# Kernel optimization log

Hardware: AMD Instinct MI355X
Metric: run time of the kernel (lower is better)

The kernel has to match this reference:

```python
import jax, jax.numpy as jnp
import numpy as np

HIDDEN = 2048
HEADS = 16
HEAD_DIM = HIDDEN // HEADS
BATCH = 2
SEQ = 2048


def setup_inputs() -> dict:
    key = jax.random.key(0)
    ks = jax.random.split(key, 9)
    s = 0.02
    return {
        "x": jax.random.normal(ks[0], (BATCH, SEQ, HIDDEN), dtype=jnp.float32),
        "Wq": jax.random.normal(ks[1], (HIDDEN, HIDDEN), dtype=jnp.float32) * s,
        "bq": jax.random.normal(ks[2], (HIDDEN,), dtype=jnp.float32) * s,
        "Wk": jax.random.normal(ks[3], (HIDDEN, HIDDEN), dtype=jnp.float32) * s,
        "bk": jax.random.normal(ks[4], (HIDDEN,), dtype=jnp.float32) * s,
        "Wv": jax.random.normal(ks[5], (HIDDEN, HIDDEN), dtype=jnp.float32) * s,
        "bv": jax.random.normal(ks[6], (HIDDEN,), dtype=jnp.float32) * s,
        "Wo": jax.random.normal(ks[7], (HIDDEN, HIDDEN), dtype=jnp.float32) * s,
        "bo": jax.random.normal(ks[8], (HIDDEN,), dtype=jnp.float32) * s,
    }


def reference(x, Wq, bq, Wk, bk, Wv, bv, Wo, bo):
    B, S, H = x.shape
    # Linear layers: y = x @ W.T + b (torch nn.Linear convention, W:[out,in])
    q = x @ Wq.T + bq
    k = x @ Wk.T + bk
    v = x @ Wv.T + bv
    # [B, S, H] -> [B, nH, S, hd]
    def split_heads(t):
        return t.reshape(B, S, HEADS, HEAD_DIM).transpose(0, 2, 1, 3)
    q, k, v = split_heads(q), split_heads(k), split_heads(v)
    scale = 1.0 / (HEAD_DIM ** 0.5)
    # NOTE: original module applies NO causal mask despite its name; be faithful.
    scores = jnp.einsum('bhqd,bhkd->bhqk', q, k) * scale
    probs = jax.nn.softmax(scores, axis=-1)
    attn = jnp.einsum('bhqk,bhkd->bhqd', probs, v)
    attn = attn.transpose(0, 2, 1, 3).reshape(B, S, H)
    return attn @ Wo.T + bo
```

## Files before the change

kernel.cpp:

```cpp
#include <hip/hip_runtime.h>
#include <hip/hip_bf16.h>
#include <stdint.h>

typedef __bf16 bf16_t;
typedef __attribute__((ext_vector_type(8))) __bf16 bf16x8;
typedef __attribute__((ext_vector_type(4))) float floatx4;

typedef __attribute__((address_space(1))) const unsigned int gu32_t;
typedef __attribute__((address_space(3))) unsigned int lu32_t;

__device__ __forceinline__ void async16(const void* g, void* l) {
    __builtin_amdgcn_global_load_lds((gu32_t*)g, (lu32_t*)l, 16, 0, 0);
}

__device__ __forceinline__ uint32_t pack2(float lo, float hi) {
    union { bf16_t h[2]; uint32_t u; } cv;
    cv.h[0] = (bf16_t)lo; cv.h[1] = (bf16_t)hi;
    return cv.u;
}

__global__ __launch_bounds__(256) void cvt_f32_bf16(const float* __restrict__ in,
                                                    bf16_t* __restrict__ out) {
    int i = (blockIdx.x * 256 + threadIdx.x) * 8;
    float4 a = *(const float4*)(in + i);
    float4 b = *(const float4*)(in + i + 4);
    bf16x8 v;
    v[0] = (bf16_t)a.x; v[1] = (bf16_t)a.y; v[2] = (bf16_t)a.z; v[3] = (bf16_t)a.w;
    v[4] = (bf16_t)b.x; v[5] = (bf16_t)b.y; v[6] = (bf16_t)b.z; v[7] = (bf16_t)b.w;
    *(bf16x8*)(out + i) = v;
}

template <bool OUT_F32, bool BIAS_ROW>
__global__ __launch_bounds__(256) void gemm_bt(const bf16_t* __restrict__ A,
                                               const bf16_t* __restrict__ B,
                                               const float* __restrict__ bias,
                                               const float* __restrict__ bias2,
                                               int nsplit,
                                               float* __restrict__ Cf,
                                               bf16_t* __restrict__ Cb,
                                               int M, int N, int K, int ldc) {
    __shared__ bf16_t As[128 * 64];
    __shared__ bf16_t Bs[128 * 64];
    const int tid = threadIdx.x;
    const int wave = tid >> 6, lane = tid & 63;
    const int quad = lane >> 4, l16 = lane & 15;
    const int wm = (wave >> 1) * 64, wn = (wave & 1) * 64;
    const int tm = blockIdx.x * 128, tn = blockIdx.y * 128;

    floatx4 acc[4][4];
#pragma unroll
    for (int i = 0; i < 4; ++i)
#pragma unroll
        for (int j = 0; j < 4; ++j) acc[i][j] = floatx4{0.f, 0.f, 0.f, 0.f};

    const bf16_t* Abase = A + (size_t)tm * K;
    const bf16_t* Bbase = B + (size_t)tn * K;
    const int sw = l16 & 7;

    for (int kk = 0; kk < K; kk += 64) {
#pragma unroll
        for (int it = 0; it < 4; ++it) {
            int chunk = it * 256 + tid;
            int r = chunk >> 3, c = chunk & 7;
            int c2 = c ^ (r & 7);
            async16(Abase + r * K + kk + c2 * 8, As + (it * 256 + wave * 64) * 8);
            async16(Bbase + r * K + kk + c2 * 8, Bs + (it * 256 + wave * 64) * 8);
        }
        __syncthreads();
#pragma unroll
        for (int ks = 0; ks < 2; ++ks) {
            bf16x8 af[4], bf[4];
#pragma unroll
            for (int mt = 0; mt < 4; ++mt)
                af[mt] = *(const bf16x8*)(As + (wm + mt * 16 + l16) * 64 +
                                          ((ks * 4 + quad) ^ sw) * 8);
#pragma unroll
            for (int nt = 0; nt < 4; ++nt)
                bf[nt] = *(const bf16x8*)(Bs + (wn + nt * 16 + l16) * 64 +
                                          ((ks * 4 + quad) ^ sw) * 8);
#pragma unroll
            for (int mt = 0; mt < 4; ++mt)
#pragma unroll
                for (int nt = 0; nt < 4; ++nt)
                    acc[mt][nt] = __builtin_amdgcn_mfma_f32_16x16x32_bf16(af[mt], bf[nt],
                                                                          acc[mt][nt], 0, 0, 0);
        }
        __syncthreads();
    }
#pragma unroll
    for (int mt = 0; mt < 4; ++mt)
#pragma unroll
        for (int nt = 0; nt < 4; ++nt)
#pragma unroll
            for (int r = 0; r < 4; ++r) {
                int row = tm + wm + mt * 16 + quad * 4 + r;
                int col = tn + wn + nt * 16 + l16;
                float bv = BIAS_ROW ? bias[row]
                                    : (col < nsplit ? bias[col] : bias2[col - nsplit]);
                float v = acc[mt][nt][r] + bv;
                if (OUT_F32) Cf[(size_t)row * ldc + col] = v;
                else Cb[(size_t)row * ldc + col] = (bf16_t)v;
            }
}

__global__ __launch_bounds__(256, 4) void flash_attn(const bf16_t* __restrict__ Qp,
                                                     const bf16_t* __restrict__ Kp,
                                                     const bf16_t* __restrict__ Vt,
                                                     bf16_t* __restrict__ O) {
    __shared__ bf16_t Ks[64 * 128];
    __shared__ bf16_t Vts[128 * 64];
    const int tid = threadIdx.x;
    const int wave = tid >> 6, lane = tid & 63;
    const int quad = lane >> 4, l16 = lane & 15;
    const int QKLD = 4096, T = 4096, S = 2048, HIDO = 2048;
    const float SL2E = 0.088388347688f * 1.44269504089f;

    const int qrow0 = blockIdx.z * S + blockIdx.x * 64;
    const int krow0 = blockIdx.z * S;
    const int hoff = blockIdx.y * 128;
    const int sw = l16 & 7;

    bf16x8 qf[4];
    const bf16_t* qptr = Qp + (size_t)(qrow0 + wave * 16 + l16) * QKLD + hoff;
#pragma unroll
    for (int ks = 0; ks < 4; ++ks) qf[ks] = *(const bf16x8*)(qptr + ks * 32 + quad * 8);

    float m_i = -3.0e38f, l_i = 0.f;
    floatx4 Oacc[8];
#pragma unroll
    for (int dt = 0; dt < 8; ++dt) Oacc[dt] = floatx4{0.f, 0.f, 0.f, 0.f};

    for (int kt = 0; kt < 32; ++kt) {
        int kb = krow0 + kt * 64;
#pragma unroll
        for (int it = 0; it < 4; ++it) {
            int chunk = it * 256 + tid;
            int r = chunk >> 4, c = chunk & 15;
            int c2 = c ^ (r & 7);
            async16(Kp + (size_t)(kb + r) * QKLD + hoff + c2 * 8,
                    Ks + (it * 256 + wave * 64) * 8);
        }
#pragma unroll
        for (int it = 0; it < 4; ++it) {
            int chunk = it * 256 + tid;
            int r = chunk >> 3, c = chunk & 7;
            int c2 = c ^ (r & 7);
            async16(Vt + (size_t)(hoff + r) * T + kb + c2 * 8,
                    Vts + (it * 256 + wave * 64) * 8);
        }
        __syncthreads();

        floatx4 sf[4];
#pragma unroll
        for (int nt = 0; nt < 4; ++nt) sf[nt] = floatx4{0.f, 0.f, 0.f, 0.f};
#pragma unroll
        for (int ks = 0; ks < 4; ++ks) {
#pragma unroll
            for (int nt = 0; nt < 4; ++nt) {
                bf16x8 a = *(const bf16x8*)(Ks + (nt * 16 + l16) * 128 +
                                            ((ks * 4 + quad) ^ sw) * 8);
                sf[nt] = __builtin_amdgcn_mfma_f32_16x16x32_bf16(a, qf[ks], sf[nt], 0, 0, 0);
            }
        }

        float mx = -3.0e38f;
#pragma unroll
        for (int nt = 0; nt < 4; ++nt)
#pragma unroll
            for (int r = 0; r < 4; ++r) mx = fmaxf(mx, sf[nt][r]);
        mx *= SL2E;
        mx = fmaxf(mx, __shfl_xor(mx, 16));
        mx = fmaxf(mx, __shfl_xor(mx, 32));
        float mnew = fmaxf(m_i, mx);
        float alpha = exp2f(m_i - mnew);
        m_i = mnew;

        float rsum = 0.f;
        uint32_t pk[8];
#pragma unroll
        for (int nt = 0; nt < 4; ++nt)
#pragma unroll
            for (int h = 0; h < 2; ++h) {
                float p0 = exp2f(sf[nt][2 * h] * SL2E - mnew);
                float p1 = exp2f(sf[nt][2 * h + 1] * SL2E - mnew);
                rsum += p0 + p1;
                pk[nt * 2 + h] = pack2(p0, p1);
            }
        rsum += __shfl_xor(rsum, 16);
        rsum += __shfl_xor(rsum, 32);
        l_i = l_i * alpha + rsum;

        float aO[4];
#pragma unroll
        for (int r = 0; r < 4; ++r) aO[r] = __shfl(alpha, quad * 4 + r);
#pragma unroll
        for (int dt = 0; dt < 8; ++dt)
#pragma unroll
            for (int r = 0; r < 4; ++r) Oacc[dt][r] *= aO[r];

        const int qsel = quad >> 1;
        const int src0 = (quad & 1) * 32 + l16;
        const int src1 = src0 + 16;
#pragma unroll
        for (int ks2 = 0; ks2 < 2; ++ks2) {
            const int rA = 4 * ks2;
            uint32_t a0 = (uint32_t)__shfl((int)pk[rA + 0], src0);
            uint32_t b0 = (uint32_t)__shfl((int)pk[rA + 2], src0);
            uint32_t a1 = (uint32_t)__shfl((int)pk[rA + 1], src0);
            uint32_t b1 = (uint32_t)__shfl((int)pk[rA + 3], src0);
            uint32_t a2 = (uint32_t)__shfl((int)pk[rA + 0], src1);
            uint32_t b2 = (uint32_t)__shfl((int)pk[rA + 2], src1);
            uint32_t a3 = (uint32_t)__shfl((int)pk[rA + 1], src1);
            uint32_t b3 = (uint32_t)__shfl((int)pk[rA + 3], src1);
            union { uint32_t u[4]; bf16x8 v; } af;
            af.u[0] = qsel ? b0 : a0;
            af.u[1] = qsel ? b1 : a1;
            af.u[2] = qsel ? b2 : a2;
            af.u[3] = qsel ? b3 : a3;
#pragma unroll
            for (int dt = 0; dt < 8; ++dt) {
                bf16x8 b = *(const bf16x8*)(Vts + (dt * 16 + l16) * 64 +
                                            ((ks2 * 4 + quad) ^ sw) * 8);
                Oacc[dt] = __builtin_amdgcn_mfma_f32_16x16x32_bf16(af.v, b, Oacc[dt], 0, 0, 0);
            }
        }
        __syncthreads();
    }
    float linv = 1.0f / l_i;
    float lO[4];
#pragma unroll
    for (int r = 0; r < 4; ++r) lO[r] = __shfl(linv, quad * 4 + r);
#pragma unroll
    for (int dt = 0; dt < 8; ++dt)
#pragma unroll
        for (int r = 0; r < 4; ++r) {
            int row = qrow0 + wave * 16 + quad * 4 + r;
            int col = hoff + dt * 16 + l16;
            O[(size_t)row * HIDO + col] = (bf16_t)(Oacc[dt][r] * lO[r]);
        }
}

extern "C" void kernel_launch(void* const* d_in, const int* in_sizes, int n_in,
                              void* d_out, int out_size, void* d_ws, size_t ws_size,
                              hipStream_t stream) {
    const float* x  = (const float*)d_in[0];
    const float* Wq = (const float*)d_in[1];
    const float* bq = (const float*)d_in[2];
    const float* Wk = (const float*)d_in[3];
    const float* bk = (const float*)d_in[4];
    const float* Wv = (const float*)d_in[5];
    const float* bv = (const float*)d_in[6];
    const float* Wo = (const float*)d_in[7];
    const float* bo = (const float*)d_in[8];
    float* out = (float*)d_out;

    const int T = 4096;
    const int H = 2048;
    bf16_t* ws  = (bf16_t*)d_ws;
    bf16_t* xb  = ws;
    bf16_t* wqb = xb  + (size_t)T * H;
    bf16_t* wkb = wqb + (size_t)H * H;
    bf16_t* wvb = wkb + (size_t)H * H;
    bf16_t* wob = wvb + (size_t)H * H;
    bf16_t* QKb = wob + (size_t)H * H;
    bf16_t* Vtb = QKb + (size_t)T * 2 * H;
    bf16_t* Ab  = Vtb + (size_t)H * T;
    size_t need = (size_t)(Ab + (size_t)T * H - ws) * sizeof(bf16_t);
    if (ws_size < need) return;

    cvt_f32_bf16<<<T * H / 2048, 256, 0, stream>>>(x, xb);
    cvt_f32_bf16<<<H * H / 2048, 256, 0, stream>>>(Wq, wqb);
    cvt_f32_bf16<<<H * H / 2048, 256, 0, stream>>>(Wk, wkb);
    cvt_f32_bf16<<<H * H / 2048, 256, 0, stream>>>(Wv, wvb);
    cvt_f32_bf16<<<H * H / 2048, 256, 0, stream>>>(Wo, wob);

    dim3 gqk(T / 128, 4096 / 128);
    gemm_bt<false, false><<<gqk, 256, 0, stream>>>(xb, wqb, bq, bk, H,
                                                   nullptr, QKb, T, 4096, H, 4096);
    dim3 gv(H / 128, T / 128);
    gemm_bt<false, true><<<gv, 256, 0, stream>>>(wvb, xb, bv, nullptr, 0,
                                                 nullptr, Vtb, H, T, H, T);

    flash_attn<<<dim3(32, 16, 2), 256, 0, stream>>>(QKb, QKb + H, Vtb, Ab);

    dim3 go(T / 128, H / 128);
    gemm_bt<true, false><<<go, 256, 0, stream>>>(Ab, wob, bo, nullptr, H,
                                                 out, nullptr, T, H, H, H);
}
```

Before: 461.1 us.

## Rewrite flash attention with 32x32x16 MFMA, two waves per block, LDS-staged output

The attention kernel switches from 16x16x32 to 32x32x16 bf16 MFMA tiles, with each of two waves owning 32 query rows instead of four waves owning 16. This cuts LDS fragment reads per FLOP and simplifies the softmax reductions and the P-fragment shuffles, which drop to a single xor-32 exchange. The output is now staged through LDS to produce coalesced row stores. The cost is fewer waves per block, larger per-wave register use (occupancy hint changed to 128 threads, 2 blocks per CU), and the same 32 KB of LDS now shared by only two waves, which may hurt latency hiding.

New measurement: 463.0 us. Within noise of the previous version (+0.4%).

```diff
diff --git a/kernel.cpp b/kernel.cpp
--- a/kernel.cpp
+++ b/kernel.cpp
@@ -5,6 +5,7 @@
 typedef __bf16 bf16_t;
 typedef __attribute__((ext_vector_type(8))) __bf16 bf16x8;
 typedef __attribute__((ext_vector_type(4))) float floatx4;
+typedef __attribute__((ext_vector_type(16))) float f32x16;
 
 typedef __attribute__((address_space(1))) const unsigned int gu32_t;
 typedef __attribute__((address_space(3))) unsigned int lu32_t;
@@ -103,141 +104,143 @@
             }
 }
 
-__global__ __launch_bounds__(256, 4) void flash_attn(const bf16_t* __restrict__ Qp,
+__global__ __launch_bounds__(128, 2) void flash_attn(const bf16_t* __restrict__ Qp,
                                                      const bf16_t* __restrict__ Kp,
                                                      const bf16_t* __restrict__ Vt,
                                                      bf16_t* __restrict__ O) {
     __shared__ bf16_t Ks[64 * 128];
     __shared__ bf16_t Vts[128 * 64];
     const int tid = threadIdx.x;
-    const int wave = tid >> 6, lane = tid & 63;
-    const int quad = lane >> 4, l16 = lane & 15;
-    const int QKLD = 4096, T = 4096, S = 2048, HIDO = 2048;
+    const int wv = tid >> 6, lane = tid & 63;
+    const int hi = lane >> 5, l32 = lane & 31;
+    const int LD = 4096, T = 4096, S = 2048, HO = 2048;
     const float SL2E = 0.088388347688f * 1.44269504089f;
 
     const int qrow0 = blockIdx.z * S + blockIdx.x * 64;
     const int krow0 = blockIdx.z * S;
     const int hoff = blockIdx.y * 128;
-    const int sw = l16 & 7;
-
-    bf16x8 qf[4];
-    const bf16_t* qptr = Qp + (size_t)(qrow0 + wave * 16 + l16) * QKLD + hoff;
-#pragma unroll
-    for (int ks = 0; ks < 4; ++ks) qf[ks] = *(const bf16x8*)(qptr + ks * 32 + quad * 8);
+    const int sw7 = l32 & 7;
+
+    bf16x8 qf[8];
+    const bf16_t* qptr = Qp + (size_t)(qrow0 + wv * 32 + l32) * LD + hoff + hi * 8;
+#pragma unroll
+    for (int ks = 0; ks < 8; ++ks) qf[ks] = *(const bf16x8*)(qptr + ks * 16);
 
     float m_i = -3.0e38f, l_i = 0.f;
-    floatx4 Oacc[8];
-#pragma unroll
-    for (int dt = 0; dt < 8; ++dt) Oacc[dt] = floatx4{0.f, 0.f, 0.f, 0.f};
+    f32x16 Oacc[4];
+#pragma unroll
+    for (int dt = 0; dt < 4; ++dt)
+#pragma unroll
+        for (int r = 0; r < 16; ++r) Oacc[dt][r] = 0.f;
 
     for (int kt = 0; kt < 32; ++kt) {
         int kb = krow0 + kt * 64;
 #pragma unroll
-        for (int it = 0; it < 4; ++it) {
-            int chunk = it * 256 + tid;
+        for (int it = 0; it < 8; ++it) {
+            int chunk = it * 128 + tid;
             int r = chunk >> 4, c = chunk & 15;
             int c2 = c ^ (r & 7);
-            async16(Kp + (size_t)(kb + r) * QKLD + hoff + c2 * 8,
-                    Ks + (it * 256 + wave * 64) * 8);
-        }
-#pragma unroll
-        for (int it = 0; it < 4; ++it) {
-            int chunk = it * 256 + tid;
+            async16(Kp + (size_t)(kb + r) * LD + hoff + c2 * 8, Ks + chunk * 8);
+        }
+#pragma unroll
+        for (int it = 0; it < 8; ++it) {
+            int chunk = it * 128 + tid;
             int r = chunk >> 3, c = chunk & 7;
             int c2 = c ^ (r & 7);
-            async16(Vt + (size_t)(hoff + r) * T + kb + c2 * 8,
-                    Vts + (it * 256 + wave * 64) * 8);
-        }
-        __syncthreads();
-
-        floatx4 sf[4];
-#pragma unroll
-        for (int nt = 0; nt < 4; ++nt) sf[nt] = floatx4{0.f, 0.f, 0.f, 0.f};
-#pragma unroll
-        for (int ks = 0; ks < 4; ++ks) {
-#pragma unroll
-            for (int nt = 0; nt < 4; ++nt) {
-                bf16x8 a = *(const bf16x8*)(Ks + (nt * 16 + l16) * 128 +
-                                            ((ks * 4 + quad) ^ sw) * 8);
-                sf[nt] = __builtin_amdgcn_mfma_f32_16x16x32_bf16(a, qf[ks], sf[nt], 0, 0, 0);
+            async16(Vt + (size_t)(hoff + r) * T + kb + c2 * 8, Vts + chunk * 8);
+        }
+        __syncthreads();
+
+        f32x16 sf[2];
+#pragma unroll
+        for (int mt = 0; mt < 2; ++mt)
+#pragma unroll
+            for (int r = 0; r < 16; ++r) sf[mt][r] = 0.f;
+#pragma unroll
+        for (int ks = 0; ks < 8; ++ks) {
+#pragma unroll
+            for (int mt = 0; mt < 2; ++mt) {
+                bf16x8 a = *(const bf16x8*)(Ks + (mt * 32 + l32) * 128 +
+                                            ((2 * ks + hi) ^ sw7) * 8);
+                sf[mt] = __builtin_amdgcn_mfma_f32_32x32x16_bf16(a, qf[ks], sf[mt], 0, 0, 0);
             }
         }
 
         float mx = -3.0e38f;
 #pragma unroll
-        for (int nt = 0; nt < 4; ++nt)
-#pragma unroll
-            for (int r = 0; r < 4; ++r) mx = fmaxf(mx, sf[nt][r]);
+        for (int mt = 0; mt < 2; ++mt)
+#pragma unroll
+            for (int r = 0; r < 16; ++r) mx = fmaxf(mx, sf[mt][r]);
+        mx = fmaxf(mx, __shfl_xor(mx, 32));
         mx *= SL2E;
-        mx = fmaxf(mx, __shfl_xor(mx, 16));
-        mx = fmaxf(mx, __shfl_xor(mx, 32));
         float mnew = fmaxf(m_i, mx);
         float alpha = exp2f(m_i - mnew);
         m_i = mnew;
 
         float rsum = 0.f;
-        uint32_t pk[8];
-#pragma unroll
-        for (int nt = 0; nt < 4; ++nt)
-#pragma unroll
-            for (int h = 0; h < 2; ++h) {
-                float p0 = exp2f(sf[nt][2 * h] * SL2E - mnew);
-                float p1 = exp2f(sf[nt][2 * h + 1] * SL2E - mnew);
-                rsum += p0 + p1;
-                pk[nt * 2 + h] = pack2(p0, p1);
-            }
-        rsum += __shfl_xor(rsum, 16);
+        uint32_t pk[16];
+#pragma unroll
+        for (int mt = 0; mt < 2; ++mt)
+#pragma unroll
+            for (int a4 = 0; a4 < 4; ++a4) {
+                float p0 = exp2f(sf[mt][4 * a4 + 0] * SL2E - mnew);
+                float p1 = exp2f(sf[mt][4 * a4 + 1] * SL2E - mnew);
+                float p2 = exp2f(sf[mt][4 * a4 + 2] * SL2E - mnew);
+                float p3 = exp2f(sf[mt][4 * a4 + 3] * SL2E - mnew);
+                rsum += (p0 + p1) + (p2 + p3);
+                pk[mt * 8 + a4 * 2 + 0] = pack2(p0, p1);
+                pk[mt * 8 + a4 * 2 + 1] = pack2(p2, p3);
+            }
         rsum += __shfl_xor(rsum, 32);
         l_i = l_i * alpha + rsum;
 
-        float aO[4];
-#pragma unroll
-        for (int r = 0; r < 4; ++r) aO[r] = __shfl(alpha, quad * 4 + r);
-#pragma unroll
-        for (int dt = 0; dt < 8; ++dt)
-#pragma unroll
-            for (int r = 0; r < 4; ++r) Oacc[dt][r] *= aO[r];
-
-        const int qsel = quad >> 1;
-        const int src0 = (quad & 1) * 32 + l16;
-        const int src1 = src0 + 16;
-#pragma unroll
-        for (int ks2 = 0; ks2 < 2; ++ks2) {
-            const int rA = 4 * ks2;
-            uint32_t a0 = (uint32_t)__shfl((int)pk[rA + 0], src0);
-            uint32_t b0 = (uint32_t)__shfl((int)pk[rA + 2], src0);
-            uint32_t a1 = (uint32_t)__shfl((int)pk[rA + 1], src0);
-            uint32_t b1 = (uint32_t)__shfl((int)pk[rA + 3], src0);
-            uint32_t a2 = (uint32_t)__shfl((int)pk[rA + 0], src1);
-            uint32_t b2 = (uint32_t)__shfl((int)pk[rA + 2], src1);
-            uint32_t a3 = (uint32_t)__shfl((int)pk[rA + 1], src1);
-            uint32_t b3 = (uint32_t)__shfl((int)pk[rA + 3], src1);
-            union { uint32_t u[4]; bf16x8 v; } af;
-            af.u[0] = qsel ? b0 : a0;
-            af.u[1] = qsel ? b1 : a1;
-            af.u[2] = qsel ? b2 : a2;
-            af.u[3] = qsel ? b3 : a3;
-#pragma unroll
-            for (int dt = 0; dt < 8; ++dt) {
-                bf16x8 b = *(const bf16x8*)(Vts + (dt * 16 + l16) * 64 +
-                                            ((ks2 * 4 + quad) ^ sw) * 8);
-                Oacc[dt] = __builtin_amdgcn_mfma_f32_16x16x32_bf16(af.v, b, Oacc[dt], 0, 0, 0);
+#pragma unroll
+        for (int dt = 0; dt < 4; ++dt)
+#pragma unroll
+            for (int r = 0; r < 16; ++r) Oacc[dt][r] *= alpha;
+
+#pragma unroll
+        for (int s = 0; s < 4; ++s) {
+            int base = (s >> 1) * 8 + (s & 1) * 4;
+            uint32_t PA0 = pk[base + 0], PA1 = pk[base + 1];
+            uint32_t PB0 = pk[base + 2], PB1 = pk[base + 3];
+            uint32_t rA0 = (uint32_t)__shfl_xor((int)PA0, 32);
+            uint32_t rA1 = (uint32_t)__shfl_xor((int)PA1, 32);
+            uint32_t rB0 = (uint32_t)__shfl_xor((int)PB0, 32);
+            uint32_t rB1 = (uint32_t)__shfl_xor((int)PB1, 32);
+            union { uint32_t u[4]; bf16x8 v; } w;
+            w.u[0] = hi ? rB0 : PA0;
+            w.u[1] = hi ? rB1 : PA1;
+            w.u[2] = hi ? PB0 : rA0;
+            w.u[3] = hi ? PB1 : rA1;
+#pragma unroll
+            for (int dt = 0; dt < 4; ++dt) {
+                bf16x8 a = *(const bf16x8*)(Vts + (dt * 32 + l32) * 64 +
+                                            ((2 * s + hi) ^ sw7) * 8);
+                Oacc[dt] = __builtin_amdgcn_mfma_f32_32x32x16_bf16(a, w.v, Oacc[dt], 0, 0, 0);
             }
         }
         __syncthreads();
     }
+
     float linv = 1.0f / l_i;
-    float lO[4];
-#pragma unroll
-    for (int r = 0; r < 4; ++r) lO[r] = __shfl(linv, quad * 4 + r);
-#pragma unroll
-    for (int dt = 0; dt < 8; ++dt)
-#pragma unroll
-        for (int r = 0; r < 4; ++r) {
-            int row = qrow0 + wave * 16 + quad * 4 + r;
-            int col = hoff + dt * 16 + l16;
-            O[(size_t)row * HIDO + col] = (bf16_t)(Oacc[dt][r] * lO[r]);
-        }
+    uint32_t* Os = (uint32_t*)Ks + wv * 2048;
+#pragma unroll
+    for (int dt = 0; dt < 4; ++dt)
+#pragma unroll
+        for (int a4 = 0; a4 < 4; ++a4) {
+            uint32_t q0 = pack2(Oacc[dt][4 * a4 + 0] * linv, Oacc[dt][4 * a4 + 1] * linv);
+            uint32_t q1 = pack2(Oacc[dt][4 * a4 + 2] * linv, Oacc[dt][4 * a4 + 3] * linv);
+            int d2 = 16 * dt + 4 * a4 + 2 * hi;
+            Os[l32 * 64 + ((d2 + 2 * l32) & 63)] = q0;
+            Os[l32 * 64 + ((d2 + 1 + 2 * l32) & 63)] = q1;
+        }
+#pragma unroll
+    for (int r = 0; r < 32; ++r) {
+        uint32_t v = Os[r * 64 + ((lane + 2 * r) & 63)];
+        uint32_t* orow = (uint32_t*)(O + (size_t)(qrow0 + wv * 32 + r) * HO + hoff);
+        orow[lane] = v;
+    }
 }
 
 extern "C" void kernel_launch(void* const* d_in, const int* in_sizes, int n_in,
@@ -281,7 +284,7 @@
     gemm_bt<false, true><<<gv, 256, 0, stream>>>(wvb, xb, bv, nullptr, 0,
                                                  nullptr, Vtb, H, T, H, T);
 
-    flash_attn<<<dim3(32, 16, 2), 256, 0, stream>>>(QKb, QKb + H, Vtb, Ab);
+    flash_attn<<<dim3(32, 16, 2), 128, 0, stream>>>(QKb, QKb + H, Vtb, Ab);
 
     dim3 go(T / 128, H / 128);
     gemm_bt<true, false><<<go, 256, 0, stream>>>(Ab, wob, bo, nullptr, H,
```
